# Performance work log

Hardware: AMD Instinct MI355X
Metric: run time of the kernel (lower is better)

Reference implementation:

```python
import jax, jax.numpy as jnp
import numpy as np

D = 2048      # input_dim
E = 64        # num_experts
TOPK = 8
N = 16384     # tokens


def setup_inputs() -> dict:
    key = jax.random.key(0)
    k_x, k_w1, k_b1, k_w2, k_b2 = jax.random.split(key, 5)
    s1 = 1.0 / np.sqrt(D)
    return {
        "x": jax.random.normal(k_x, (N, D), dtype=jnp.float32),
        "W1": jax.random.uniform(k_w1, (D, D), minval=-s1, maxval=s1, dtype=jnp.float32),
        "b1": jax.random.uniform(k_b1, (D,), minval=-s1, maxval=s1, dtype=jnp.float32),
        "W2": jax.random.uniform(k_w2, (D, E), minval=-s1, maxval=s1, dtype=jnp.float32),
        "b2": jax.random.uniform(k_b2, (E,), minval=-s1, maxval=s1, dtype=jnp.float32),
    }


def reference(x, W1, b1, W2, b2):
    # gate MLP: Linear -> GELU (exact, erf-based as torch nn.GELU default) -> Linear
    h = jax.nn.gelu(x @ W1 + b1, approximate=False)
    logits = h @ W2 + b2                              # [N, E]
    # eval mode: no noise added
    top_vals, top_idx = jax.lax.top_k(logits, TOPK)   # [N, K]
    top_w = jax.nn.softmax(top_vals, axis=-1)         # softmax over selected logits
    rows = jnp.arange(logits.shape[0])[:, None]       # [N, 1]
    routing_weights = jnp.zeros_like(logits).at[rows, top_idx].set(top_w)
    # load balance loss
    probs = jax.nn.softmax(logits, axis=-1)
    freq = (routing_weights > 0).astype(logits.dtype).mean(axis=0)   # [E]
    avg_prob = probs.mean(axis=0)                                    # [E]
    load_balance_loss = E * jnp.sum(freq * avg_prob)
    return routing_weights, top_idx, load_balance_loss
```

## Files before the change

kernel.cpp:

```cpp
#include <hip/hip_runtime.h>
#include <math.h>
#include <stdint.h>

#define N_TOK 16384
#define DIM   2048
#define NEXP  64
#define TOPK  8

#define BM 128
#define BN 128
#define BKE 32

typedef _Float16 half8 __attribute__((ext_vector_type(8)));
typedef _Float16 half4 __attribute__((ext_vector_type(4)));
typedef float    f32x4 __attribute__((ext_vector_type(4)));

#define GLOBAL_AS __attribute__((address_space(1)))
#define LDS_AS    __attribute__((address_space(3)))

#define LO_SCALE     4096.0f
#define INV_LO_SCALE (1.0f / 4096.0f)

__device__ inline uint32_t pack_split(float v) {
    _Float16 hi = (_Float16)v;
    float r = (v - (float)hi) * LO_SCALE;
    _Float16 lo = (_Float16)r;
    return (uint32_t)__builtin_bit_cast(uint16_t, hi) |
           ((uint32_t)__builtin_bit_cast(uint16_t, lo) << 16);
}

__device__ inline _Float16 split_hi(float v) { return (_Float16)v; }
__device__ inline _Float16 split_lo(float v) {
    _Float16 hi = (_Float16)v;
    return (_Float16)((v - (float)hi) * LO_SCALE);
}

union U4H8 { uint32_t u[4]; half8 h; };

__device__ inline void load_frag(const uint32_t* base, int row, int quad,
                                 half8& hi, half8& lo) {
    const int sw = row & 7;
    const uint4 q0 = *(const uint4*)(base + row * 32 + (((quad * 2)     ^ sw) << 2));
    const uint4 q1 = *(const uint4*)(base + row * 32 + (((quad * 2 + 1) ^ sw) << 2));
    uint32_t u[8] = {q0.x, q0.y, q0.z, q0.w, q1.x, q1.y, q1.z, q1.w};
    U4H8 H, L;
    #pragma unroll
    for (int j = 0; j < 4; j++) {
        H.u[j] = (u[2 * j] & 0xffffu) | (u[2 * j + 1] << 16);
        L.u[j] = (u[2 * j] >> 16)     | (u[2 * j + 1] & 0xffff0000u);
    }
    hi = H.h; lo = L.h;
}

__device__ inline void load_frag2(const _Float16* base, int row, int quad,
                                  half8& hi, half8& lo) {
    const int sw = row & 7;
    hi = *(const half8*)(base + row * 64 + ((quad       ^ sw) << 3));
    lo = *(const half8*)(base + row * 64 + (((quad + 4) ^ sw) << 3));
}

__global__ __launch_bounds__(256) void convert_x_split(
    const float* __restrict__ x, _Float16* __restrict__ xhi,
    _Float16* __restrict__ xlo)
{
    size_t i = ((size_t)blockIdx.x * 256 + threadIdx.x) * 8;
    float4 v0 = *(const float4*)(x + i);
    float4 v1 = *(const float4*)(x + i + 4);
    const float vv[8] = {v0.x, v0.y, v0.z, v0.w, v1.x, v1.y, v1.z, v1.w};
    half8 h, l;
    #pragma unroll
    for (int j = 0; j < 8; j++) { h[j] = split_hi(vv[j]); l[j] = split_lo(vv[j]); }
    *(half8*)(xhi + i) = h;
    *(half8*)(xlo + i) = l;
}

__global__ __launch_bounds__(256) void convert_w1t_split(
    const float* __restrict__ W1, _Float16* __restrict__ w1hi,
    _Float16* __restrict__ w1lo)
{
    __shared__ float s[32][33];
    const int k0 = blockIdx.y * 32, n0 = blockIdx.x * 32;
    const int tr = threadIdx.x & 31, tc = threadIdx.x >> 5;
    #pragma unroll
    for (int r = 0; r < 4; r++) {
        int row = tc + r * 8;
        s[row][tr] = W1[(size_t)(k0 + row) * DIM + n0 + tr];
    }
    __syncthreads();
    #pragma unroll
    for (int r = 0; r < 4; r++) {
        int row = tc + r * 8;
        float v = s[tr][row];
        w1hi[(size_t)(n0 + row) * DIM + k0 + tr] = split_hi(v);
        w1lo[(size_t)(n0 + row) * DIM + k0 + tr] = split_lo(v);
    }
}

__global__ __launch_bounds__(256) void convert_w2t(const float* __restrict__ W2,
                                                   uint32_t* __restrict__ W2Tp) {
    int i = blockIdx.x * 256 + threadIdx.x;
    int e = i >> 11, n = i & 2047;
    W2Tp[i] = pack_split(W2[(size_t)n * NEXP + e]);
}

__global__ __launch_bounds__(256) void convert_x_inplace(float* __restrict__ x) {
    size_t i = ((size_t)blockIdx.x * 256 + threadIdx.x) * 4;
    float4 v = *(const float4*)(x + i);
    uint4 p;
    p.x = pack_split(v.x); p.y = pack_split(v.y);
    p.z = pack_split(v.z); p.w = pack_split(v.w);
    *(uint4*)(x + i) = p;
}

__global__ __launch_bounds__(256) void convert_w1t_packed(
    const float* __restrict__ W1, uint32_t* __restrict__ W1Tp)
{
    __shared__ float s[32][33];
    const int k0 = blockIdx.y * 32, n0 = blockIdx.x * 32;
    const int tr = threadIdx.x & 31, tc = threadIdx.x >> 5;
    #pragma unroll
    for (int r = 0; r < 4; r++) {
        int row = tc + r * 8;
        s[row][tr] = W1[(size_t)(k0 + row) * DIM + n0 + tr];
    }
    __syncthreads();
    #pragma unroll
    for (int r = 0; r < 4; r++) {
        int row = tc + r * 8;
        W1Tp[(size_t)(n0 + row) * DIM + k0 + tr] = pack_split(s[tr][row]);
    }
}


#define KSTEP(ASrc_, BSrc_, ASt_, BSt_, DOSTAGE_)                               \
    {                                                                           \
        if (DOSTAGE_) {                                                         \
            _Pragma("unroll")                                                   \
            for (int r = 0; r < 4; r++) {                                       \
                const int wslot = (r * 256 + wid * 64) << 2;                    \
                __builtin_amdgcn_global_load_lds(                               \
                    (const GLOBAL_AS uint32_t*)gA[r],                           \
                    (LDS_AS uint32_t*)((ASt_) + wslot), 16, 0, 0);              \
                __builtin_amdgcn_global_load_lds(                               \
                    (const GLOBAL_AS uint32_t*)gB[r],                           \
                    (LDS_AS uint32_t*)((BSt_) + wslot), 16, 0, 0);              \
                gA[r] += BKE; gB[r] += BKE;                                     \
            }                                                                   \
        }                                                                       \
        half8 ah[4], al[4], bh[4], bl[4];                                       \
        _Pragma("unroll")                                                       \
        for (int mt = 0; mt < 4; mt++)                                          \
            load_frag2((const _Float16*)(ASrc_), wm + mt * 16 + l16, quad,      \
                       ah[mt], al[mt]);                                         \
        _Pragma("unroll")                                                       \
        for (int nt = 0; nt < 4; nt++)                                          \
            load_frag2((const _Float16*)(BSrc_), wn + nt * 16 + l16, quad,      \
                       bh[nt], bl[nt]);                                         \
        __builtin_amdgcn_s_setprio(1);                                          \
        _Pragma("unroll")                                                       \
        for (int mt = 0; mt < 4; mt++)                                          \
            _Pragma("unroll")                                                   \
            for (int nt = 0; nt < 4; nt++) {                                    \
                am[mt][nt] = __builtin_amdgcn_mfma_f32_16x16x32_f16(            \
                    ah[mt], bh[nt], am[mt][nt], 0, 0, 0);                       \
                ac[mt][nt] = __builtin_amdgcn_mfma_f32_16x16x32_f16(            \
                    ah[mt], bl[nt], ac[mt][nt], 0, 0, 0);                       \
                ac[mt][nt] = __builtin_amdgcn_mfma_f32_16x16x32_f16(            \
                    al[mt], bh[nt], ac[mt][nt], 0, 0, 0);                       \
            }                                                                   \
        __builtin_amdgcn_s_setprio(0);                                          \
        __syncthreads();                                                        \
    }

__global__ __launch_bounds__(256, 2) void gemm_fused_v2(
    const _Float16* __restrict__ xhi, const _Float16* __restrict__ xlo,
    const _Float16* __restrict__ w1hi, const _Float16* __restrict__ w1lo,
    const float* __restrict__ b1, const uint32_t* __restrict__ W2Tp,
    float* __restrict__ Lp)
{
    __shared__ uint32_t smem[16384];
    uint32_t* A0 = smem;
    uint32_t* B0 = smem + 4096;
    uint32_t* A1 = smem + 8192;
    uint32_t* B1 = smem + 12288;

    const int t    = threadIdx.x;
    const int wid  = t >> 6;
    const int lane = t & 63;
    const int quad = lane >> 4;
    const int l16  = lane & 15;

    const int lin = blockIdx.x;
    const int grp = lin >> 7;
    const int rem = lin & 127;
    const int m0 = (grp * 8 + (rem & 7)) * BM;
    const int n0 = (rem >> 3) * BN;

    const _Float16* gA[4];
    const _Float16* gB[4];
    #pragma unroll
    for (int r = 0; r < 4; r++) {
        int s_lin = r * 256 + t;
        int row = s_lin >> 3;
        int c   = (s_lin & 7) ^ (row & 7);
        gA[r] = (c < 4) ? xhi  + (size_t)(m0 + row) * DIM + c * 8
                        : xlo  + (size_t)(m0 + row) * DIM + (c - 4) * 8;
        gB[r] = (c < 4) ? w1hi + (size_t)(n0 + row) * DIM + c * 8
                        : w1lo + (size_t)(n0 + row) * DIM + (c - 4) * 8;
    }

    f32x4 am[4][4], ac[4][4];
    #pragma unroll
    for (int i = 0; i < 4; i++)
        #pragma unroll
        for (int j = 0; j < 4; j++) { am[i][j] = (f32x4)0.0f; ac[i][j] = (f32x4)0.0f; }

    const int wm = (wid & 1) * 64;
    const int wn = (wid >> 1) * 64;

    #pragma unroll
    for (int r = 0; r < 4; r++) {
        const int wslot = (r * 256 + wid * 64) << 2;
        __builtin_amdgcn_global_load_lds((const GLOBAL_AS uint32_t*)gA[r],
                                         (LDS_AS uint32_t*)(A0 + wslot), 16, 0, 0);
        __builtin_amdgcn_global_load_lds((const GLOBAL_AS uint32_t*)gB[r],
                                         (LDS_AS uint32_t*)(B0 + wslot), 16, 0, 0);
        gA[r] += BKE; gB[r] += BKE;
    }
    __syncthreads();

    for (int kp = 0; kp < 32; kp++) {
        KSTEP(A0, B0, A1, B1, true);
        KSTEP(A1, B1, A0, B0, kp != 31);
    }

    uint32_t* Hs = smem;
    #pragma unroll
    for (int mt = 0; mt < 4; mt++)
        #pragma unroll
        for (int nt = 0; nt < 4; nt++) {
            const int coln = wn + nt * 16 + l16;
            const float b1v = b1[n0 + coln];
            #pragma unroll
            for (int r = 0; r < 4; r++) {
                float h = am[mt][nt][r] + ac[mt][nt][r] * INV_LO_SCALE + b1v;
                h = 0.5f * h * (1.0f + erff(h * 0.70710678118654752440f));
                const int rowm = wm + mt * 16 + quad * 4 + r;
                const int word = rowm * 128 + ((((coln >> 2) ^ (rowm & 7)) << 2) | (coln & 3));
                Hs[word] = pack_split(h);
            }
        }
    __syncthreads();

    f32x4 a2m[2][4], a2c[2][4];
    #pragma unroll
    for (int i = 0; i < 2; i++)
        #pragma unroll
        for (int j = 0; j < 4; j++) { a2m[i][j] = (f32x4)0.0f; a2c[i][j] = (f32x4)0.0f; }

    #pragma unroll
    for (int ks = 0; ks < 4; ks++) {
        half8 a2h[2], a2l[2];
        #pragma unroll
        for (int mt2 = 0; mt2 < 2; mt2++) {
            const int row = wid * 32 + mt2 * 16 + l16;
            const int sw  = row & 7;
            const int cb  = ks * 8 + quad * 2;
            const uint4 q0 = *(const uint4*)(Hs + row * 128 + ((cb ^ sw) << 2));
            const uint4 q1 = *(const uint4*)(Hs + row * 128 + (((cb + 1) ^ sw) << 2));
            uint32_t u[8] = {q0.x, q0.y, q0.z, q0.w, q1.x, q1.y, q1.z, q1.w};
            U4H8 H, L;
            #pragma unroll
            for (int j = 0; j < 4; j++) {
                H.u[j] = (u[2 * j] & 0xffffu) | (u[2 * j + 1] << 16);
                L.u[j] = (u[2 * j] >> 16)     | (u[2 * j + 1] & 0xffff0000u);
            }
            a2h[mt2] = H.h; a2l[mt2] = L.h;
        }
        #pragma unroll
        for (int et = 0; et < 4; et++) {
            const int e = et * 16 + l16;
            const uint32_t* wp = W2Tp + (size_t)e * DIM + n0 + ks * 32 + quad * 8;
            const uint4 q0 = *(const uint4*)wp;
            const uint4 q1 = *(const uint4*)(wp + 4);
            uint32_t u[8] = {q0.x, q0.y, q0.z, q0.w, q1.x, q1.y, q1.z, q1.w};
            U4H8 H, L;
            #pragma unroll
            for (int j = 0; j < 4; j++) {
                H.u[j] = (u[2 * j] & 0xffffu) | (u[2 * j + 1] << 16);
                L.u[j] = (u[2 * j] >> 16)     | (u[2 * j + 1] & 0xffff0000u);
            }
            #pragma unroll
            for (int mt2 = 0; mt2 < 2; mt2++) {
                a2m[mt2][et] = __builtin_amdgcn_mfma_f32_16x16x32_f16(a2h[mt2], H.h, a2m[mt2][et], 0, 0, 0);
                a2c[mt2][et] = __builtin_amdgcn_mfma_f32_16x16x32_f16(a2h[mt2], L.h, a2c[mt2][et], 0, 0, 0);
                a2c[mt2][et] = __builtin_amdgcn_mfma_f32_16x16x32_f16(a2l[mt2], H.h, a2c[mt2][et], 0, 0, 0);
            }
        }
    }

    #pragma unroll
    for (int mt2 = 0; mt2 < 2; mt2++)
        #pragma unroll
        for (int et = 0; et < 4; et++)
            #pragma unroll
            for (int r = 0; r < 4; r++) {
                const float lg = a2m[mt2][et][r] + a2c[mt2][et][r] * INV_LO_SCALE;
                const int rowm = m0 + wid * 32 + mt2 * 16 + quad * 4 + r;
                const int e = et * 16 + l16;
                atomicAdd(&Lp[(size_t)rowm * NEXP + e], lg);
            }
}

__global__ __launch_bounds__(256, 2) void gemm_fused(
    const uint32_t* __restrict__ xp, const uint32_t* __restrict__ W1Tp,
    const float* __restrict__ b1, const uint32_t* __restrict__ W2Tp,
    float* __restrict__ Lp)
{
    __shared__ uint32_t smem[16384];
    uint32_t* Ap = smem;
    uint32_t* Bp = smem + 4096;

    const int t    = threadIdx.x;
    const int wid  = t >> 6;
    const int lane = t & 63;
    const int quad = lane >> 4;
    const int l16  = lane & 15;

    const int lin = blockIdx.x;
    const int grp = lin >> 7;
    const int rem = lin & 127;
    const int m0 = (grp * 8 + (rem & 7)) * BM;
    const int n0 = (rem >> 3) * BN;

    const uint32_t* gA[4];
    const uint32_t* gB[4];
    #pragma unroll
    for (int r = 0; r < 4; r++) {
        int s = r * 256 + t;
        int row = s >> 3;
        int c   = s & 7;
        int co  = (c ^ (row & 7)) << 2;
        gA[r] = xp   + (size_t)(m0 + row) * DIM + co;
        gB[r] = W1Tp + (size_t)(n0 + row) * DIM + co;
    }

    f32x4 am[4][4], ac[4][4];
    #pragma unroll
    for (int i = 0; i < 4; i++)
        #pragma unroll
        for (int j = 0; j < 4; j++) { am[i][j] = (f32x4)0.0f; ac[i][j] = (f32x4)0.0f; }

    const int wm = (wid & 1) * 64;
    const int wn = (wid >> 1) * 64;

    for (int k0 = 0; k0 < DIM; k0 += BKE) {
        #pragma unroll
        for (int r = 0; r < 4; r++) {
            const int wslot = (r * 256 + wid * 64) << 2;
            __builtin_amdgcn_global_load_lds((const GLOBAL_AS uint32_t*)gA[r],
                                             (LDS_AS uint32_t*)(Ap + wslot), 16, 0, 0);
            __builtin_amdgcn_global_load_lds((const GLOBAL_AS uint32_t*)gB[r],
                                             (LDS_AS uint32_t*)(Bp + wslot), 16, 0, 0);
            gA[r] += BKE; gB[r] += BKE;
        }
        __syncthreads();

        half8 ah[4], al[4], bh[4], bl[4];
        #pragma unroll
        for (int mt = 0; mt < 4; mt++)
            load_frag(Ap, wm + mt * 16 + l16, quad, ah[mt], al[mt]);
        #pragma unroll
        for (int nt = 0; nt < 4; nt++)
            load_frag(Bp, wn + nt * 16 + l16, quad, bh[nt], bl[nt]);

        #pragma unroll
        for (int mt = 0; mt < 4; mt++)
            #pragma unroll
            for (int nt = 0; nt < 4; nt++) {
                am[mt][nt] = __builtin_amdgcn_mfma_f32_16x16x32_f16(ah[mt], bh[nt], am[mt][nt], 0, 0, 0);
                ac[mt][nt] = __builtin_amdgcn_mfma_f32_16x16x32_f16(ah[mt], bl[nt], ac[mt][nt], 0, 0, 0);
                ac[mt][nt] = __builtin_amdgcn_mfma_f32_16x16x32_f16(al[mt], bh[nt], ac[mt][nt], 0, 0, 0);
            }
        __syncthreads();
    }

    uint32_t* Hs = smem;
    #pragma unroll
    for (int mt = 0; mt < 4; mt++)
        #pragma unroll
        for (int nt = 0; nt < 4; nt++) {
            const int coln = wn + nt * 16 + l16;
            const float b1v = b1[n0 + coln];
            #pragma unroll
            for (int r = 0; r < 4; r++) {
                float h = am[mt][nt][r] + ac[mt][nt][r] * INV_LO_SCALE + b1v;
                h = 0.5f * h * (1.0f + erff(h * 0.70710678118654752440f));
                const int rowm = wm + mt * 16 + quad * 4 + r;
                const int word = rowm * 128 + ((((coln >> 2) ^ (rowm & 7)) << 2) | (coln & 3));
                Hs[word] = pack_split(h);
            }
        }
    __syncthreads();

    f32x4 a2m[2][4], a2c[2][4];
    #pragma unroll
    for (int i = 0; i < 2; i++)
        #pragma unroll
        for (int j = 0; j < 4; j++) { a2m[i][j] = (f32x4)0.0f; a2c[i][j] = (f32x4)0.0f; }

    #pragma unroll
    for (int ks = 0; ks < 4; ks++) {
        half8 a2h[2], a2l[2];
        #pragma unroll
        for (int mt2 = 0; mt2 < 2; mt2++) {
            const int row = wid * 32 + mt2 * 16 + l16;
            const int sw  = row & 7;
            const int cb  = ks * 8 + quad * 2;
            const uint4 q0 = *(const uint4*)(Hs + row * 128 + ((cb ^ sw) << 2));
            const uint4 q1 = *(const uint4*)(Hs + row * 128 + (((cb + 1) ^ sw) << 2));
            uint32_t u[8] = {q0.x, q0.y, q0.z, q0.w, q1.x, q1.y, q1.z, q1.w};
            U4H8 H, L;
            #pragma unroll
            for (int j = 0; j < 4; j++) {
                H.u[j] = (u[2 * j] & 0xffffu) | (u[2 * j + 1] << 16);
                L.u[j] = (u[2 * j] >> 16)     | (u[2 * j + 1] & 0xffff0000u);
            }
            a2h[mt2] = H.h; a2l[mt2] = L.h;
        }
        #pragma unroll
        for (int et = 0; et < 4; et++) {
            const int e = et * 16 + l16;
            const uint32_t* wp = W2Tp + (size_t)e * DIM + n0 + ks * 32 + quad * 8;
            const uint4 q0 = *(const uint4*)wp;
            const uint4 q1 = *(const uint4*)(wp + 4);
            uint32_t u[8] = {q0.x, q0.y, q0.z, q0.w, q1.x, q1.y, q1.z, q1.w};
            U4H8 H, L;
            #pragma unroll
            for (int j = 0; j < 4; j++) {
                H.u[j] = (u[2 * j] & 0xffffu) | (u[2 * j + 1] << 16);
                L.u[j] = (u[2 * j] >> 16)     | (u[2 * j + 1] & 0xffff0000u);
            }
            #pragma unroll
            for (int mt2 = 0; mt2 < 2; mt2++) {
                a2m[mt2][et] = __builtin_amdgcn_mfma_f32_16x16x32_f16(a2h[mt2], H.h, a2m[mt2][et], 0, 0, 0);
                a2c[mt2][et] = __builtin_amdgcn_mfma_f32_16x16x32_f16(a2h[mt2], L.h, a2c[mt2][et], 0, 0, 0);
                a2c[mt2][et] = __builtin_amdgcn_mfma_f32_16x16x32_f16(a2l[mt2], H.h, a2c[mt2][et], 0, 0, 0);
            }
        }
    }

    #pragma unroll
    for (int mt2 = 0; mt2 < 2; mt2++)
        #pragma unroll
        for (int et = 0; et < 4; et++)
            #pragma unroll
            for (int r = 0; r < 4; r++) {
                const float lg = a2m[mt2][et][r] + a2c[mt2][et][r] * INV_LO_SCALE;
                const int rowm = m0 + wid * 32 + mt2 * 16 + quad * 4 + r;
                const int e = et * 16 + l16;
                atomicAdd(&Lp[(size_t)rowm * NEXP + e], lg);
            }
}

__global__ __launch_bounds__(256) void router_topk_v2(
    const float* __restrict__ Lp, const float* __restrict__ b2,
    float* __restrict__ out_rw, float* __restrict__ out_idx,
    float* __restrict__ gP, float* __restrict__ gI)
{
    __shared__ float sP[NEXP];
    __shared__ float sI[NEXP];
    const int t = threadIdx.x;
    if (t < NEXP) { sP[t] = 0.f; sI[t] = 0.f; }
    __syncthreads();

    const int lane = t & 63;
    const int wv   = t >> 6;
    const float b2v = b2[lane];

    float accP = 0.f, accSel = 0.f;

    for (int i = 0; i < 16; i++) {
        const int tok = blockIdx.x * 64 + i * 4 + wv;
        float logit = Lp[(size_t)tok * NEXP + lane] + b2v;

        float mx = logit;
        #pragma unroll
        for (int off = 32; off >= 1; off >>= 1) mx = fmaxf(mx, __shfl_xor(mx, off));
        float p = expf(logit - mx);
        float ps = p;
        #pragma unroll
        for (int off = 32; off >= 1; off >>= 1) ps += __shfl_xor(ps, off);
        accP += p / ps;

        float cur = logit;
        float tv[TOPK]; int tix[TOPK];
        for (int k = 0; k < TOPK; k++) {
            float v = cur; int idx = lane;
            #pragma unroll
            for (int off = 32; off >= 1; off >>= 1) {
                float ov = __shfl_xor(v, off);
                int   oi = __shfl_xor(idx, off);
                if (ov > v || (ov == v && oi < idx)) { v = ov; idx = oi; }
            }
            tv[k] = v; tix[k] = idx;
            if (lane == idx) cur = -INFINITY;
        }

        float ev[TOPK], s = 0.f;
        #pragma unroll
        for (int k = 0; k < TOPK; k++) { ev[k] = expf(tv[k] - tv[0]); s += ev[k]; }
        float w = 0.f;
        #pragma unroll
        for (int k = 0; k < TOPK; k++)
            if (tix[k] == lane) { w = ev[k] / s; accSel += 1.f; }

        out_rw[(size_t)tok * NEXP + lane] = w;
        if (lane < TOPK) out_idx[(size_t)tok * TOPK + lane] = (float)tix[lane];
    }

    atomicAdd(&sP[lane], accP);
    atomicAdd(&sI[lane], accSel);
    __syncthreads();
    if (t < NEXP) { atomicAdd(&gP[t], sP[t]); atomicAdd(&gI[t], sI[t]); }
}

__global__ void loss_kernel(const float* __restrict__ gP,
                            const float* __restrict__ gI,
                            float* __restrict__ out_loss)
{
    const int lane = threadIdx.x;
    const float inv = 1.0f / (float)N_TOK;
    float v = (gI[lane] * inv) * (gP[lane] * inv);
    #pragma unroll
    for (int off = 32; off >= 1; off >>= 1) v += __shfl_xor(v, off);
    if (lane == 0) out_loss[0] = (float)NEXP * v;
}

extern "C" void kernel_launch(void* const* d_in, const int* in_sizes, int n_in,
                              void* d_out, int out_size, void* d_ws, size_t ws_size,
                              hipStream_t stream) {
    const float* x  = (const float*)d_in[0];
    const float* W1 = (const float*)d_in[1];
    const float* b1 = (const float*)d_in[2];
    const float* W2 = (const float*)d_in[3];
    const float* b2 = (const float*)d_in[4];

    float* out_rw   = (float*)d_out;
    float* out_idx  = out_rw + (size_t)N_TOK * NEXP;
    float* out_loss = out_idx + (size_t)N_TOK * TOPK;

    const size_t SZ_X   = (size_t)N_TOK * DIM * 2;
    const size_t SZ_W1  = (size_t)DIM * DIM * 2;
    const size_t OFF_XHI   = 0;
    const size_t OFF_XLO   = OFF_XHI + SZ_X;
    const size_t OFF_W1HI  = OFF_XLO + SZ_X;
    const size_t OFF_W1LO  = OFF_W1HI + SZ_W1;
    const size_t OFF_W2T   = OFF_W1LO + SZ_W1;
    const size_t OFF_LP    = OFF_W2T + (size_t)DIM * NEXP * 4;
    const size_t OFF_G     = OFF_LP + (size_t)N_TOK * NEXP * 4;
    const size_t needed_v2 = OFF_G + 2 * NEXP * 4;

    const size_t P_W1T = 0;
    const size_t P_W2T = (size_t)16 << 20;
    const size_t P_LP  = (size_t)17 << 20;
    const size_t P_G   = P_LP + (size_t)N_TOK * NEXP * 4;
    const size_t needed_p = P_G + 2 * NEXP * 4;

    if (ws_size >= needed_v2) {
        _Float16* xhi  = (_Float16*)((char*)d_ws + OFF_XHI);
        _Float16* xlo  = (_Float16*)((char*)d_ws + OFF_XLO);
        _Float16* w1hi = (_Float16*)((char*)d_ws + OFF_W1HI);
        _Float16* w1lo = (_Float16*)((char*)d_ws + OFF_W1LO);
        uint32_t* W2Tp = (uint32_t*)((char*)d_ws + OFF_W2T);
        float* Lp = (float*)((char*)d_ws + OFF_LP);
        float* gP = (float*)((char*)d_ws + OFF_G);
        float* gI = gP + NEXP;

        (void)hipMemsetAsync((char*)d_ws + OFF_LP, 0,
                             (size_t)N_TOK * NEXP * 4 + 2 * NEXP * 4, stream);
        convert_x_split  <<<(N_TOK * DIM) / (256 * 8), 256, 0, stream>>>(x, xhi, xlo);
        convert_w1t_split<<<dim3(DIM / 32, DIM / 32), 256, 0, stream>>>(W1, w1hi, w1lo);
        convert_w2t      <<<(NEXP * DIM) / 256, 256, 0, stream>>>(W2, W2Tp);
        gemm_fused_v2<<<(N_TOK / BM) * (DIM / BN), 256, 0, stream>>>(
            xhi, xlo, w1hi, w1lo, b1, W2Tp, Lp);
        router_topk_v2<<<N_TOK / 64, 256, 0, stream>>>(Lp, b2, out_rw, out_idx, gP, gI);
        loss_kernel<<<1, 64, 0, stream>>>(gP, gI, out_loss);
    } else if (ws_size >= needed_p) {
        uint32_t* W1Tp = (uint32_t*)((char*)d_ws + P_W1T);
        uint32_t* W2Tp = (uint32_t*)((char*)d_ws + P_W2T);
        float* Lp = (float*)((char*)d_ws + P_LP);
        float* gP = (float*)((char*)d_ws + P_G);
        float* gI = gP + NEXP;

        (void)hipMemsetAsync((char*)d_ws + P_LP, 0,
                             (size_t)N_TOK * NEXP * 4 + 2 * NEXP * 4, stream);
        convert_x_inplace<<<(N_TOK * DIM) / (256 * 4), 256, 0, stream>>>((float*)d_in[0]);
        convert_w1t_packed<<<dim3(DIM / 32, DIM / 32), 256, 0, stream>>>(W1, W1Tp);
        convert_w2t<<<(NEXP * DIM) / 256, 256, 0, stream>>>(W2, W2Tp);
        gemm_fused<<<(N_TOK / BM) * (DIM / BN), 256, 0, stream>>>(
            (const uint32_t*)d_in[0], W1Tp, b1, W2Tp, Lp);
        router_topk_v2<<<N_TOK / 64, 256, 0, stream>>>(Lp, b2, out_rw, out_idx, gP, gI);
        loss_kernel<<<1, 64, 0, stream>>>(gP, gI, out_loss);
    }
}
```

Baseline: 739.4 us.

## Split GEMM k-step into two LDS/MFMA halves, merge converts and loss kernel

The GEMM inner step now loads half the A fragments and all B fragments before issuing the next global-to-LDS stage. It then runs MFMAs on that half while loading the second half, using explicit s_barrier and waitcnt in place of a single __syncthreads. This is meant to overlap LDS reads with MFMA work and global prefetch. Separately, the three conversion kernels are merged into one launch, and the loss kernel is folded into the router via a last-block ticket, which removes launch overhead but adds atomics and fence ordering risk.

```diff
diff --git a/kernel.cpp b/kernel.cpp
--- a/kernel.cpp
+++ b/kernel.cpp
@@ -59,48 +59,51 @@
     lo = *(const half8*)(base + row * 64 + (((quad + 4) ^ sw) << 3));
 }
 
-__global__ __launch_bounds__(256) void convert_x_split(
-    const float* __restrict__ x, _Float16* __restrict__ xhi,
-    _Float16* __restrict__ xlo)
+#define CVT_XBLKS  ((N_TOK * DIM) / (256 * 8))
+#define CVT_W1BLKS ((DIM / 32) * (DIM / 32))
+#define CVT_W2BLKS ((NEXP * DIM) / 256)
+
+__global__ __launch_bounds__(256) void convert_all(
+    const float* __restrict__ x, const float* __restrict__ W1,
+    const float* __restrict__ W2,
+    _Float16* __restrict__ xhi, _Float16* __restrict__ xlo,
+    _Float16* __restrict__ w1hi, _Float16* __restrict__ w1lo,
+    uint32_t* __restrict__ W2Tp)
 {
-    size_t i = ((size_t)blockIdx.x * 256 + threadIdx.x) * 8;
-    float4 v0 = *(const float4*)(x + i);
-    float4 v1 = *(const float4*)(x + i + 4);
-    const float vv[8] = {v0.x, v0.y, v0.z, v0.w, v1.x, v1.y, v1.z, v1.w};
-    half8 h, l;
-    #pragma unroll
-    for (int j = 0; j < 8; j++) { h[j] = split_hi(vv[j]); l[j] = split_lo(vv[j]); }
-    *(half8*)(xhi + i) = h;
-    *(half8*)(xlo + i) = l;
-}
-
-__global__ __launch_bounds__(256) void convert_w1t_split(
-    const float* __restrict__ W1, _Float16* __restrict__ w1hi,
-    _Float16* __restrict__ w1lo)
-{
-    __shared__ float s[32][33];
-    const int k0 = blockIdx.y * 32, n0 = blockIdx.x * 32;
-    const int tr = threadIdx.x & 31, tc = threadIdx.x >> 5;
-    #pragma unroll
-    for (int r = 0; r < 4; r++) {
-        int row = tc + r * 8;
-        s[row][tr] = W1[(size_t)(k0 + row) * DIM + n0 + tr];
-    }
-    __syncthreads();
-    #pragma unroll
-    for (int r = 0; r < 4; r++) {
-        int row = tc + r * 8;
-        float v = s[tr][row];
-        w1hi[(size_t)(n0 + row) * DIM + k0 + tr] = split_hi(v);
-        w1lo[(size_t)(n0 + row) * DIM + k0 + tr] = split_lo(v);
-    }
-}
-
-__global__ __launch_bounds__(256) void convert_w2t(const float* __restrict__ W2,
-                                                   uint32_t* __restrict__ W2Tp) {
-    int i = blockIdx.x * 256 + threadIdx.x;
-    int e = i >> 11, n = i & 2047;
-    W2Tp[i] = pack_split(W2[(size_t)n * NEXP + e]);
+    const int b = blockIdx.x;
+    if (b < CVT_XBLKS) {
+        size_t i = ((size_t)b * 256 + threadIdx.x) * 8;
+        float4 v0 = *(const float4*)(x + i);
+        float4 v1 = *(const float4*)(x + i + 4);
+        const float vv[8] = {v0.x, v0.y, v0.z, v0.w, v1.x, v1.y, v1.z, v1.w};
+        half8 h, l;
+        #pragma unroll
+        for (int j = 0; j < 8; j++) { h[j] = split_hi(vv[j]); l[j] = split_lo(vv[j]); }
+        *(half8*)(xhi + i) = h;
+        *(half8*)(xlo + i) = l;
+    } else if (b < CVT_XBLKS + CVT_W1BLKS) {
+        __shared__ float s[32][33];
+        const int bb = b - CVT_XBLKS;
+        const int n0 = (bb & 63) * 32, k0 = (bb >> 6) * 32;
+        const int tr = threadIdx.x & 31, tc = threadIdx.x >> 5;
+        #pragma unroll
+        for (int r = 0; r < 4; r++) {
+            int row = tc + r * 8;
+            s[row][tr] = W1[(size_t)(k0 + row) * DIM + n0 + tr];
+        }
+        __syncthreads();
+        #pragma unroll
+        for (int r = 0; r < 4; r++) {
+            int row = tc + r * 8;
+            float v = s[tr][row];
+            w1hi[(size_t)(n0 + row) * DIM + k0 + tr] = split_hi(v);
+            w1lo[(size_t)(n0 + row) * DIM + k0 + tr] = split_lo(v);
+        }
+    } else {
+        const int i = (b - CVT_XBLKS - CVT_W1BLKS) * 256 + threadIdx.x;
+        const int e = i >> 11, n = i & 2047;
+        W2Tp[i] = pack_split(W2[(size_t)n * NEXP + e]);
+    }
 }
 
 __global__ __launch_bounds__(256) void convert_x_inplace(float* __restrict__ x) {
@@ -131,9 +134,37 @@
     }
 }
 
+__global__ __launch_bounds__(256) void convert_w2t_packed(
+    const float* __restrict__ W2, uint32_t* __restrict__ W2Tp) {
+    int i = blockIdx.x * 256 + threadIdx.x;
+    int e = i >> 11, n = i & 2047;
+    W2Tp[i] = pack_split(W2[(size_t)n * NEXP + e]);
+}
+
+
+#define ASM_VMCNT0() asm volatile("s_waitcnt vmcnt(0)" ::: "memory")
+#define ASM_LGKM0()  asm volatile("s_waitcnt lgkmcnt(0)" ::: "memory")
+
+#define MFMA3(mt_, nt_)                                                         \
+    am[mt_][nt_] = __builtin_amdgcn_mfma_f32_16x16x32_f16(                      \
+        ah[mt_], bh[nt_], am[mt_][nt_], 0, 0, 0);                               \
+    ac[mt_][nt_] = __builtin_amdgcn_mfma_f32_16x16x32_f16(                      \
+        ah[mt_], bl[nt_], ac[mt_][nt_], 0, 0, 0);                               \
+    ac[mt_][nt_] = __builtin_amdgcn_mfma_f32_16x16x32_f16(                      \
+        al[mt_], bh[nt_], ac[mt_][nt_], 0, 0, 0);
 
 #define KSTEP(ASrc_, BSrc_, ASt_, BSt_, DOSTAGE_)                               \
     {                                                                           \
+        half8 ah[4], al[4], bh[4], bl[4];                                       \
+            \
+        _Pragma("unroll")                                                       \
+        for (int mt = 0; mt < 2; mt++)                                          \
+            load_frag2((const _Float16*)(ASrc_), wm + mt * 16 + l16, quad,      \
+                       ah[mt], al[mt]);                                         \
+        _Pragma("unroll")                                                       \
+        for (int nt = 0; nt < 4; nt++)                                          \
+            load_frag2((const _Float16*)(BSrc_), wn + nt * 16 + l16, quad,      \
+                       bh[nt], bl[nt]);                                         \
         if (DOSTAGE_) {                                                         \
             _Pragma("unroll")                                                   \
             for (int r = 0; r < 4; r++) {                                       \
@@ -147,29 +178,30 @@
                 gA[r] += BKE; gB[r] += BKE;                                     \
             }                                                                   \
         }                                                                       \
-        half8 ah[4], al[4], bh[4], bl[4];                                       \
+        __builtin_amdgcn_s_barrier();                                           \
+        ASM_LGKM0();                                                            \
+        __builtin_amdgcn_s_setprio(1);                                          \
         _Pragma("unroll")                                                       \
-        for (int mt = 0; mt < 4; mt++)                                          \
+        for (int mt = 0; mt < 2; mt++)                                          \
+            _Pragma("unroll")                                                   \
+            for (int nt = 0; nt < 4; nt++) { MFMA3(mt, nt) }                    \
+        __builtin_amdgcn_s_setprio(0);                                          \
+        __builtin_amdgcn_s_barrier();                                           \
+                                      \
+        _Pragma("unroll")                                                       \
+        for (int mt = 2; mt < 4; mt++)                                          \
             load_frag2((const _Float16*)(ASrc_), wm + mt * 16 + l16, quad,      \
                        ah[mt], al[mt]);                                         \
-        _Pragma("unroll")                                                       \
-        for (int nt = 0; nt < 4; nt++)                                          \
-            load_frag2((const _Float16*)(BSrc_), wn + nt * 16 + l16, quad,      \
-                       bh[nt], bl[nt]);                                         \
+        __builtin_amdgcn_s_barrier();                                           \
+        ASM_LGKM0();                                                            \
         __builtin_amdgcn_s_setprio(1);                                          \
         _Pragma("unroll")                                                       \
-        for (int mt = 0; mt < 4; mt++)                                          \
+        for (int mt = 2; mt < 4; mt++)                                          \
             _Pragma("unroll")                                                   \
-            for (int nt = 0; nt < 4; nt++) {                                    \
-                am[mt][nt] = __builtin_amdgcn_mfma_f32_16x16x32_f16(            \
-                    ah[mt], bh[nt], am[mt][nt], 0, 0, 0);                       \
-                ac[mt][nt] = __builtin_amdgcn_mfma_f32_16x16x32_f16(            \
-                    ah[mt], bl[nt], ac[mt][nt], 0, 0, 0);                       \
-                ac[mt][nt] = __builtin_amdgcn_mfma_f32_16x16x32_f16(            \
-                    al[mt], bh[nt], ac[mt][nt], 0, 0, 0);                       \
-            }                                                                   \
+            for (int nt = 0; nt < 4; nt++) { MFMA3(mt, nt) }                    \
         __builtin_amdgcn_s_setprio(0);                                          \
-        __syncthreads();                                                        \
+        ASM_VMCNT0();           \
+        __builtin_amdgcn_s_barrier();                                           \
     }
 
 __global__ __launch_bounds__(256, 2) void gemm_fused_v2(
@@ -227,7 +259,8 @@
                                          (LDS_AS uint32_t*)(B0 + wslot), 16, 0, 0);
         gA[r] += BKE; gB[r] += BKE;
     }
-    __syncthreads();
+    ASM_VMCNT0();
+    __builtin_amdgcn_s_barrier();
 
     for (int kp = 0; kp < 32; kp++) {
         KSTEP(A0, B0, A1, B1, true);
@@ -463,13 +496,15 @@
             }
 }
 
-__global__ __launch_bounds__(256) void router_topk_v2(
+__global__ __launch_bounds__(256) void router_topk_v3(
     const float* __restrict__ Lp, const float* __restrict__ b2,
     float* __restrict__ out_rw, float* __restrict__ out_idx,
-    float* __restrict__ gP, float* __restrict__ gI)
+    float* __restrict__ gP, float* __restrict__ gI,
+    float* __restrict__ out_loss, uint32_t* __restrict__ done)
 {
     __shared__ float sP[NEXP];
     __shared__ float sI[NEXP];
+    __shared__ uint32_t ticket;
     const int t = threadIdx.x;
     if (t < NEXP) { sP[t] = 0.f; sI[t] = 0.f; }
     __syncthreads();
@@ -523,18 +558,22 @@
     atomicAdd(&sI[lane], accSel);
     __syncthreads();
     if (t < NEXP) { atomicAdd(&gP[t], sP[t]); atomicAdd(&gI[t], sI[t]); }
-}
-
-__global__ void loss_kernel(const float* __restrict__ gP,
-                            const float* __restrict__ gI,
-                            float* __restrict__ out_loss)
-{
-    const int lane = threadIdx.x;
-    const float inv = 1.0f / (float)N_TOK;
-    float v = (gI[lane] * inv) * (gP[lane] * inv);
-    #pragma unroll
-    for (int off = 32; off >= 1; off >>= 1) v += __shfl_xor(v, off);
-    if (lane == 0) out_loss[0] = (float)NEXP * v;
+
+    __threadfence();
+    if (t == 0) ticket = atomicAdd(done, 1u);
+    __syncthreads();
+    if (ticket == (uint32_t)(gridDim.x - 1)) {
+        __threadfence();
+        if (t < NEXP) {
+            const float inv = 1.0f / (float)N_TOK;
+            float fI = atomicAdd(&gI[t], 0.0f);
+            float fP = atomicAdd(&gP[t], 0.0f);
+            float v = (fI * inv) * (fP * inv);
+            #pragma unroll
+            for (int off = 32; off >= 1; off >>= 1) v += __shfl_xor(v, off);
+            if (t == 0) out_loss[0] = (float)NEXP * v;
+        }
+    }
 }
 
 extern "C" void kernel_launch(void* const* d_in, const int* in_sizes, int n_in,
@@ -559,13 +598,13 @@
     const size_t OFF_W2T   = OFF_W1LO + SZ_W1;
     const size_t OFF_LP    = OFF_W2T + (size_t)DIM * NEXP * 4;
     const size_t OFF_G     = OFF_LP + (size_t)N_TOK * NEXP * 4;
-    const size_t needed_v2 = OFF_G + 2 * NEXP * 4;
+    const size_t needed_v2 = OFF_G + 2 * NEXP * 4 + 16;
 
     const size_t P_W1T = 0;
     const size_t P_W2T = (size_t)16 << 20;
     const size_t P_LP  = (size_t)17 << 20;
     const size_t P_G   = P_LP + (size_t)N_TOK * NEXP * 4;
-    const size_t needed_p = P_G + 2 * NEXP * 4;
+    const size_t needed_p = P_G + 2 * NEXP * 4 + 16;
 
     if (ws_size >= needed_v2) {
         _Float16* xhi  = (_Float16*)((char*)d_ws + OFF_XHI);
@@ -576,31 +615,32 @@
         float* Lp = (float*)((char*)d_ws + OFF_LP);
         float* gP = (float*)((char*)d_ws + OFF_G);
         float* gI = gP + NEXP;
+        uint32_t* done = (uint32_t*)(gI + NEXP);
 
         (void)hipMemsetAsync((char*)d_ws + OFF_LP, 0,
-                             (size_t)N_TOK * NEXP * 4 + 2 * NEXP * 4, stream);
-        convert_x_split  <<<(N_TOK * DIM) / (256 * 8), 256, 0, stream>>>(x, xhi, xlo);
-        convert_w1t_split<<<dim3(DIM / 32, DIM / 32), 256, 0, stream>>>(W1, w1hi, w1lo);
-        convert_w2t      <<<(NEXP * DIM) / 256, 256, 0, stream>>>(W2, W2Tp);
+                             (size_t)N_TOK * NEXP * 4 + 2 * NEXP * 4 + 16, stream);
+        convert_all<<<CVT_XBLKS + CVT_W1BLKS + CVT_W2BLKS, 256, 0, stream>>>(
+            x, W1, W2, xhi, xlo, w1hi, w1lo, W2Tp);
         gemm_fused_v2<<<(N_TOK / BM) * (DIM / BN), 256, 0, stream>>>(
             xhi, xlo, w1hi, w1lo, b1, W2Tp, Lp);
-        router_topk_v2<<<N_TOK / 64, 256, 0, stream>>>(Lp, b2, out_rw, out_idx, gP, gI);
-        loss_kernel<<<1, 64, 0, stream>>>(gP, gI, out_loss);
+        router_topk_v3<<<N_TOK / 64, 256, 0, stream>>>(
+            Lp, b2, out_rw, out_idx, gP, gI, out_loss, done);
     } else if (ws_size >= needed_p) {
         uint32_t* W1Tp = (uint32_t*)((char*)d_ws + P_W1T);
         uint32_t* W2Tp = (uint32_t*)((char*)d_ws + P_W2T);
         float* Lp = (float*)((char*)d_ws + P_LP);
         float* gP = (float*)((char*)d_ws + P_G);
         float* gI = gP + NEXP;
+        uint32_t* done = (uint32_t*)(gI + NEXP);
 
         (void)hipMemsetAsync((char*)d_ws + P_LP, 0,
-                             (size_t)N_TOK * NEXP * 4 + 2 * NEXP * 4, stream);
+                             (size_t)N_TOK * NEXP * 4 + 2 * NEXP * 4 + 16, stream);
         convert_x_inplace<<<(N_TOK * DIM) / (256 * 4), 256, 0, stream>>>((float*)d_in[0]);
         convert_w1t_packed<<<dim3(DIM / 32, DIM / 32), 256, 0, stream>>>(W1, W1Tp);
-        convert_w2t<<<(NEXP * DIM) / 256, 256, 0, stream>>>(W2, W2Tp);
+        convert_w2t_packed<<<(NEXP * DIM) / 256, 256, 0, stream>>>(W2, W2Tp);
         gemm_fused<<<(N_TOK / BM) * (DIM / BN), 256, 0, stream>>>(
             (const uint32_t*)d_in[0], W1Tp, b1, W2Tp, Lp);
-        router_topk_v2<<<N_TOK / 64, 256, 0, stream>>>(Lp, b2, out_rw, out_idx, gP, gI);
-        loss_kernel<<<1, 64, 0, stream>>>(gP, gI, out_loss);
-    }
-}
+        router_topk_v3<<<N_TOK / 64, 256, 0, stream>>>(
+            Lp, b2, out_rw, out_idx, gP, gI, out_loss, done);
+    }
+}
```

Result: slower. 767.2 us (+3.8%).
